# Kernel optimization log

Hardware: AMD Instinct MI355X
Metric: run time of the kernel (lower is better)

Reference implementation:

```python
import jax, jax.numpy as jnp
import numpy as np

T, B, X, F, Z, H = 64, 512, 784, 64, 64, 512


def _lin(v, W, b):
    return v @ W.T + b


def _gru(xt, h, Wih, Whh, bih, bhh):
    # PyTorch GRUCell gate math
    gi = xt @ Wih.T + bih
    gh = h @ Whh.T + bhh
    ir, iz, in_ = jnp.split(gi, 3, axis=-1)
    hr, hz, hn = jnp.split(gh, 3, axis=-1)
    r = jax.nn.sigmoid(ir + hr)
    z = jax.nn.sigmoid(iz + hz)
    n = jnp.tanh(in_ + r * hn)
    return (1.0 - z) * n + z * h


def _kld(mu1, sd1, mu2, sd2):
    r = sd1 / sd2
    return 0.5 * jnp.sum(((mu1 - mu2) / sd2) ** 2 + r ** 2 - 2.0 * jnp.log(r) - 1.0)


def setup_inputs() -> dict:
    key = jax.random.key(0)
    ks = iter(jax.random.split(key, 64))

    def Wn(*shape):
        return 0.02 * jax.random.normal(next(ks), shape, jnp.float32)

    d = {}
    d["x"] = jax.random.uniform(next(ks), (T, B, X), jnp.float32)
    d["eps_f"] = jax.random.normal(next(ks), (B, F), jnp.float32)
    d["eps_z"] = jax.random.normal(next(ks), (T, B, Z), jnp.float32)
    d.update(
        pxW1=Wn(H, X), pxb1=Wn(H), pxW2=Wn(H, H), pxb2=Wn(H),
        pzW=Wn(H, Z), pzb=Wn(H),
        pfW=Wn(H, F), pfb=Wn(H),
        rWih=Wn(3 * H, 3 * H), rWhh=Wn(3 * H, H), rbih=Wn(3 * H), rbhh=Wn(3 * H),
        zpW=Wn(H, H), zpb=Wn(H), zpmW=Wn(Z, H), zpmb=Wn(Z), zpsW=Wn(Z, H), zpsb=Wn(Z),
        feWih=Wn(3 * H, H), feWhh=Wn(3 * H, H), febih=Wn(3 * H), febhh=Wn(3 * H),
        femW=Wn(F, H), femb=Wn(F), fesW=Wn(F, H), fesb=Wn(F),
        zeW1=Wn(H, 2 * H), zeb1=Wn(H), zeW2=Wn(H, H), zeb2=Wn(H),
        zemW=Wn(Z, H), zemb=Wn(Z), zesW=Wn(Z, H), zesb=Wn(Z),
        dW1=Wn(H, 3 * H), db1=Wn(H), dW2=Wn(H, H), db2=Wn(H),
        dmW=Wn(X, H), dmb=Wn(X),
    )
    return d


def reference(x, eps_f, eps_z, pxW1, pxb1, pxW2, pxb2, pzW, pzb, pfW, pfb,
              rWih, rWhh, rbih, rbhh, zpW, zpb, zpmW, zpmb, zpsW, zpsb,
              feWih, feWhh, febih, febhh, femW, femb, fesW, fesb,
              zeW1, zeb1, zeW2, zeb2, zemW, zemb, zesW, zesb,
              dW1, db1, dW2, db2, dmW, dmb):
    relu = jax.nn.relu
    # phi_x over all timesteps at once: [T, B, H]
    phi_x = relu(_lin(relu(_lin(x, pxW1, pxb1)), pxW2, pxb2))
    h0 = jnp.zeros((x.shape[1], H), x.dtype)

    # f encoder GRU over the sequence; only the final hidden is used
    f_h, _ = jax.lax.scan(
        lambda h, xt: (_gru(xt, h, feWih, feWhh, febih, febhh), None), h0, phi_x)
    f_mean = _lin(f_h, femW, femb)
    f_std = jax.nn.softplus(_lin(f_h, fesW, fesb))
    f = eps_f * f_std + f_mean
    phi_f = relu(_lin(f, pfW, pfb))
    f_kld = _kld(f_mean, f_std, jnp.zeros_like(f_mean), jnp.ones_like(f_std))

    def step(carry, inp):
        h, zk, nll = carry
        px_t, e_t, x_t = inp
        zp = relu(_lin(h, zpW, zpb))
        zpm = _lin(zp, zpmW, zpmb)
        zps = jax.nn.softplus(_lin(zp, zpsW, zpsb))
        ze = relu(_lin(relu(_lin(jnp.concatenate([px_t, h], 1), zeW1, zeb1)), zeW2, zeb2))
        zem = _lin(ze, zemW, zemb)
        zes = jax.nn.softplus(_lin(ze, zesW, zesb))
        z_t = e_t * zes + zem
        phi_z = relu(_lin(z_t, pzW, pzb))
        dec = relu(_lin(relu(_lin(jnp.concatenate([phi_z, phi_f, h], 1), dW1, db1)), dW2, db2))
        dec_mean = jax.nn.sigmoid(_lin(dec, dmW, dmb))
        h_new = _gru(jnp.concatenate([px_t, phi_z, phi_f], 1), h, rWih, rWhh, rbih, rbhh)
        zk = zk + _kld(zem, zes, zpm, zps)
        nll = nll - jnp.sum(x_t * jnp.log(dec_mean) + (1.0 - x_t) * jnp.log(1.0 - dec_mean))
        return (h_new, zk, nll), None

    zero = jnp.zeros((), x.dtype)
    (_, z_kld, nll), _ = jax.lax.scan(step, (h0, zero, zero), (phi_x, eps_z, x))
    return (f_kld, z_kld, nll)
```

## Files before the change

### kernel.cpp

```cpp
#include <hip/hip_runtime.h>
#include <cmath>

namespace {

constexpr int Tn = 64;
constexpr int Bn = 512;
constexpr int Xn = 784;
constexpr int XnP = 800;
constexpr int Fn = 64;
constexpr int Zn = 64;
constexpr int Hn = 512;

typedef unsigned short us;
typedef __attribute__((ext_vector_type(8))) short bf16x8;
typedef __attribute__((ext_vector_type(4))) float f32x4;

__device__ __forceinline__ us f2b(float v) {
  unsigned int u = __float_as_uint(v);
  return (us)((u + 0x7FFFu + ((u >> 16) & 1u)) >> 16);
}
__device__ __forceinline__ float b2f(us u) { return __uint_as_float(((unsigned int)u) << 16); }
__device__ __forceinline__ float sigmf(float v) { return 1.0f / (1.0f + __expf(-v)); }
__device__ __forceinline__ float splusf(float v) {
  return v > 0.0f ? (v + log1pf(__expf(-v))) : log1pf(__expf(v));
}
__device__ __forceinline__ float block_sum(float v, float* red) {
  #pragma unroll
  for (int off = 32; off > 0; off >>= 1) v += __shfl_down(v, off, 64);
  if ((threadIdx.x & 63) == 0) red[threadIdx.x >> 6] = v;
  __syncthreads();
  float s = 0.0f;
  if (threadIdx.x == 0) s = red[0] + red[1] + red[2] + red[3];
  return s;
}

__global__ void cvt(const float* __restrict__ s, us* __restrict__ d, int n) {
  int i = blockIdx.x * 256 + threadIdx.x;
  if (i < n) d[i] = f2b(s[i]);
}
__global__ void cvt_pad(const float* __restrict__ s, us* __restrict__ d, int C, int Cp, int n) {
  int i = blockIdx.x * 256 + threadIdx.x;
  if (i < n) {
    int r = i / Cp, c = i - r * Cp;
    d[i] = (c < C) ? f2b(s[(size_t)r * C + c]) : (us)0;
  }
}

template <int NSEG, bool RELU, bool F32OUT, bool HASINIT, bool HASBIAS>
__device__ void tile_gemmx(
    int bx, int by,
    const us* A0, const us* W0, int ldw0, int K0,
    const us* A1, const us* W1, int ldw1, int K1,
    const float* initC, int ldi, const float* bias,
    void* Cout, int ldc, char* smemc)
{
  us* As = (us*)smemc; us* Bs = (us*)(smemc + 5120);
  const int tid = threadIdx.x, srow = tid >> 2, scb = (tid & 3) * 8;
  const int lane = tid & 63, w = tid >> 6, l15 = lane & 15, q = lane >> 4;
  const int m0 = by * 64, n0 = bx * 64;
  f32x4 acc[4];
  if (HASINIT) {
    #pragma unroll
    for (int j = 0; j < 4; ++j)
      #pragma unroll
      for (int r = 0; r < 4; ++r)
        acc[j][r] = initC[(size_t)(m0 + w * 16 + q * 4 + r) * ldi + n0 + j * 16 + l15];
  } else {
    #pragma unroll
    for (int j = 0; j < 4; ++j) acc[j] = (f32x4){0.f, 0.f, 0.f, 0.f};
  }
  #pragma unroll
  for (int seg = 0; seg < NSEG; ++seg) {
    const us* A = (seg == 0) ? A0 : A1;
    const us* W = (seg == 0) ? W0 : W1;
    const int ldw = (seg == 0) ? ldw0 : ldw1;
    const int K   = (seg == 0) ? K0 : K1;
    const us* ap = A + (size_t)(m0 + srow) * K + scb;
    const us* wp = W + (size_t)(n0 + srow) * ldw + scb;
    uint4 av = *(const uint4*)ap;
    uint4 wv = *(const uint4*)wp;
    for (int k0 = 0; k0 < K; k0 += 32) {
      __syncthreads();
      *(uint4*)&As[srow * 40 + scb] = av;
      *(uint4*)&Bs[srow * 40 + scb] = wv;
      __syncthreads();
      if (k0 + 32 < K) {
        av = *(const uint4*)(ap + k0 + 32);
        wv = *(const uint4*)(wp + k0 + 32);
      }
      bf16x8 a = *(const bf16x8*)&As[(w * 16 + l15) * 40 + q * 8];
      #pragma unroll
      for (int j = 0; j < 4; ++j) {
        bf16x8 b = *(const bf16x8*)&Bs[(j * 16 + l15) * 40 + q * 8];
        acc[j] = __builtin_amdgcn_mfma_f32_16x16x32_bf16(a, b, acc[j], 0, 0, 0);
      }
    }
  }
  #pragma unroll
  for (int j = 0; j < 4; ++j) {
    const int col = n0 + j * 16 + l15;
    const float bv = HASBIAS ? bias[col] : 0.f;
    #pragma unroll
    for (int r = 0; r < 4; ++r) {
      const int row = m0 + w * 16 + q * 4 + r;
      float v = acc[j][r] + bv;
      if (RELU) v = fmaxf(v, 0.f);
      if (F32OUT) ((float*)Cout)[(size_t)row * ldc + col] = v;
      else        ((us*)Cout)[(size_t)row * ldc + col] = f2b(v);
    }
  }
}

__device__ void tile_gru_fe(
    int bx, int by,
    const us* A0, const us* Wih,
    const us* hprev, const us* Whh,
    const float* bih, const float* bhh,
    us* hnew, char* smemc)
{
  us* Asm = (us*)smemc; us* Rs = (us*)(smemc + 5120);
  us* Zs = (us*)(smemc + 10240); us* Ns = (us*)(smemc + 15360);
  const int tid = threadIdx.x, srow = tid >> 2, scb = (tid & 3) * 8;
  const int lane = tid & 63, w = tid >> 6, l15 = lane & 15, q = lane >> 4;
  const int m0 = by * 64, c0 = bx * 64;
  f32x4 aR[4], aZ[4], aI[4], aH[4];
  #pragma unroll
  for (int j = 0; j < 4; ++j) {
    aR[j] = (f32x4){0.f, 0.f, 0.f, 0.f}; aZ[j] = aR[j]; aI[j] = aR[j]; aH[j] = aR[j];
  }
  #pragma unroll
  for (int seg = 0; seg < 2; ++seg) {
    const bool hseg = (seg == 1);
    const us* A  = hseg ? hprev : A0;
    const us* Wb = hseg ? Whh : Wih;
    const us* ap = A + (size_t)(m0 + srow) * Hn + scb;
    const us* wr = Wb + (size_t)(c0 + srow) * Hn + scb;
    const us* wz = wr + (size_t)Hn * Hn;
    const us* wn = wz + (size_t)Hn * Hn;
    uint4 av = *(const uint4*)ap;
    uint4 rv = *(const uint4*)wr;
    uint4 zv = *(const uint4*)wz;
    uint4 nv = *(const uint4*)wn;
    for (int k0 = 0; k0 < Hn; k0 += 32) {
      __syncthreads();
      *(uint4*)&Asm[srow * 40 + scb] = av;
      *(uint4*)&Rs[srow * 40 + scb] = rv;
      *(uint4*)&Zs[srow * 40 + scb] = zv;
      *(uint4*)&Ns[srow * 40 + scb] = nv;
      __syncthreads();
      if (k0 + 32 < Hn) {
        av = *(const uint4*)(ap + k0 + 32);
        rv = *(const uint4*)(wr + k0 + 32);
        zv = *(const uint4*)(wz + k0 + 32);
        nv = *(const uint4*)(wn + k0 + 32);
      }
      bf16x8 a = *(const bf16x8*)&Asm[(w * 16 + l15) * 40 + q * 8];
      #pragma unroll
      for (int j = 0; j < 4; ++j) {
        bf16x8 br = *(const bf16x8*)&Rs[(j * 16 + l15) * 40 + q * 8];
        bf16x8 bz = *(const bf16x8*)&Zs[(j * 16 + l15) * 40 + q * 8];
        bf16x8 bn = *(const bf16x8*)&Ns[(j * 16 + l15) * 40 + q * 8];
// ... 51 lines not shown
    }
  }
  const us* ap = phiz + (size_t)(m0 + srow) * Hn + scb;
  const us* wr = rWih + (size_t)(c0 + srow) * 1536 + 512 + scb;
  const us* wz = wr + (size_t)512 * 1536;
  const us* wn = wz + (size_t)512 * 1536;
  uint4 av = *(const uint4*)ap;
  uint4 rv = *(const uint4*)wr;
  uint4 zv = *(const uint4*)wz;
  uint4 nv = *(const uint4*)wn;
  for (int k0 = 0; k0 < Hn; k0 += 32) {
    __syncthreads();
    *(uint4*)&Asm[srow * 40 + scb] = av;
    *(uint4*)&Rs[srow * 40 + scb] = rv;
    *(uint4*)&Zs[srow * 40 + scb] = zv;
    *(uint4*)&Ns[srow * 40 + scb] = nv;
    __syncthreads();
    if (k0 + 32 < Hn) {
      av = *(const uint4*)(ap + k0 + 32);
      rv = *(const uint4*)(wr + k0 + 32);
      zv = *(const uint4*)(wz + k0 + 32);
      nv = *(const uint4*)(wn + k0 + 32);
    }
    bf16x8 a = *(const bf16x8*)&Asm[(w * 16 + l15) * 40 + q * 8];
    #pragma unroll
    for (int j = 0; j < 4; ++j) {
      bf16x8 br = *(const bf16x8*)&Rs[(j * 16 + l15) * 40 + q * 8];
      bf16x8 bz = *(const bf16x8*)&Zs[(j * 16 + l15) * 40 + q * 8];
      bf16x8 bn = *(const bf16x8*)&Ns[(j * 16 + l15) * 40 + q * 8];
      aR[j] = __builtin_amdgcn_mfma_f32_16x16x32_bf16(a, br, aR[j], 0, 0, 0);
      aZ[j] = __builtin_amdgcn_mfma_f32_16x16x32_bf16(a, bz, aZ[j], 0, 0, 0);
      aI[j] = __builtin_amdgcn_mfma_f32_16x16x32_bf16(a, bn, aI[j], 0, 0, 0);
    }
  }
  #pragma unroll
  for (int j = 0; j < 4; ++j) {
    const int c = c0 + j * 16 + l15;
    const float bR = bih[c] + bhh[c];
    const float bZ = bih[Hn + c] + bhh[Hn + c];
    const float bI = bih[2 * Hn + c];
    const float bH = bhh[2 * Hn + c];
    #pragma unroll
    for (int r = 0; r < 4; ++r) {
      const int m = m0 + w * 16 + q * 4 + r;
      const float h = b2f(hprev[(size_t)m * Hn + c]);
      const float rg = sigmf(aR[j][r] + bR);
      const float zg = sigmf(aZ[j][r] + bZ);
      const float ng = tanhf(aI[j][r] + bI + rg * (aH[j][r] + bH));
      hnew[(size_t)m * Hn + c] = f2b((1.0f - zg) * ng + zg * h);
    }
  }
}

__device__ void tile_nll(
    int bx, int by,
    const us* dec, const us* dmW, const float* dmb, const float* xt,
    float* nll, char* smemc)
{
  us* As = (us*)smemc; us* Bs = (us*)(smemc + 5120);
  float* red = (float*)(smemc + 10240);
  const int tid = threadIdx.x, srow = tid >> 2, scb = (tid & 3) * 8;
  const int lane = tid & 63, w = tid >> 6, l15 = lane & 15, q = lane >> 4;
  const int m0 = by * 64, n0 = bx * 64;
  f32x4 acc[4];
  #pragma unroll
  for (int j = 0; j < 4; ++j) acc[j] = (f32x4){0.f, 0.f, 0.f, 0.f};
  const int wrow = (n0 + srow < Xn) ? (n0 + srow) : (Xn - 1);
  const us* ap = dec + (size_t)(m0 + srow) * Hn + scb;
  const us* wp = dmW + (size_t)wrow * Hn + scb;
  uint4 av = *(const uint4*)ap;
  uint4 wv = *(const uint4*)wp;
  for (int k0 = 0; k0 < Hn; k0 += 32) {
    __syncthreads();
    *(uint4*)&As[srow * 40 + scb] = av;
    *(uint4*)&Bs[srow * 40 + scb] = wv;
    __syncthreads();
    if (k0 + 32 < Hn) {
      av = *(const uint4*)(ap + k0 + 32);
      wv = *(const uint4*)(wp + k0 + 32);
    }
    bf16x8 a = *(const bf16x8*)&As[(w * 16 + l15) * 40 + q * 8];
    #pragma unroll
    for (int j = 0; j < 4; ++j) {
      bf16x8 b = *(const bf16x8*)&Bs[(j * 16 + l15) * 40 + q * 8];
      acc[j] = __builtin_amdgcn_mfma_f32_16x16x32_bf16(a, b, acc[j], 0, 0, 0);
    }
  }
  float sum = 0.0f;
  #pragma unroll
  for (int j = 0; j < 4; ++j) {
    const int n = n0 + j * 16 + l15;
    if (n < Xn) {
      const float bv = dmb[n];
      #pragma unroll
      for (int r = 0; r < 4; ++r) {
        const int m = m0 + w * 16 + q * 4 + r;
        const float a = acc[j][r] + bv;
        const float xv = xt[(size_t)m * Xn + n];
        sum += splusf(-a) + (1.0f - xv) * a;
      }
    }
  }
  const float s = block_sum(sum, red);
  if (tid == 0) atomicAdd(nll, s);
}

template <int MODE>
__device__ void stat_dual(int vb,
    const us* Ain, const us* Wm, const float* bm, const us* Ws, const float* bs,
    const float* eps, const float* pm_in, const float* ps_in,
    us* o0b, float* o_pm, float* o_ps, float* kacc, char* smemc)
{
  us* As = (us*)smemc; us* Ms = (us*)(smemc + 5120); us* Ss = (us*)(smemc + 10240);
  float* red = (float*)(smemc + 15360);
  const int tid = threadIdx.x, srow = tid >> 2, scb = (tid & 3) * 8;
  const int lane = tid & 63, w = tid >> 6, l15 = lane & 15, q = lane >> 4;
  const int m0 = vb * 64;
  f32x4 am[4], as_[4];
  #pragma unroll
  for (int j = 0; j < 4; ++j) { am[j] = (f32x4){0.f, 0.f, 0.f, 0.f}; as_[j] = am[j]; }
  const us* ap = Ain + (size_t)(m0 + srow) * Hn + scb;
  const us* mp = Wm + (size_t)srow * Hn + scb;
  const us* sp = Ws + (size_t)srow * Hn + scb;
  uint4 av = *(const uint4*)ap;
  uint4 mv = *(const uint4*)mp;
  uint4 sv = *(const uint4*)sp;
  for (int k0 = 0; k0 < Hn; k0 += 32) {
    __syncthreads();
    *(uint4*)&As[srow * 40 + scb] = av;
    *(uint4*)&Ms[srow * 40 + scb] = mv;
    *(uint4*)&Ss[srow * 40 + scb] = sv;
    __syncthreads();
    if (k0 + 32 < Hn) {
      av = *(const uint4*)(ap + k0 + 32);
      mv = *(const uint4*)(mp + k0 + 32);
      sv = *(const uint4*)(sp + k0 + 32);
    }
    bf16x8 a = *(const bf16x8*)&As[(w * 16 + l15) * 40 + q * 8];
    #pragma unroll
    for (int j = 0; j < 4; ++j) {
      bf16x8 b0 = *(const bf16x8*)&Ms[(j * 16 + l15) * 40 + q * 8];
      bf16x8 b1 = *(const bf16x8*)&Ss[(j * 16 + l15) * 40 + q * 8];
      am[j]  = __builtin_amdgcn_mfma_f32_16x16x32_bf16(a, b0, am[j], 0, 0, 0);
      as_[j] = __builtin_amdgcn_mfma_f32_16x16x32_bf16(a, b1, as_[j], 0, 0, 0);
    }
  }
  float kld = 0.0f;
  #pragma unroll
  for (int j = 0; j < 4; ++j) {
    const int c = j * 16 + l15;
    const float bmv = bm[c], bsv = bs[c];
    #pragma unroll
    for (int r = 0; r < 4; ++r) {
      const int m = m0 + w * 16 + q * 4 + r;
      const float mu = am[j][r] + bmv;
      const float sd = splusf(as_[j][r] + bsv);
      if (MODE == 0) {
        o_pm[(size_t)m * Zn + c] = mu;
        o_ps[(size_t)m * Zn + c] = sd;
      } else {
        o0b[(size_t)m * Zn + c] = f2b(eps[(size_t)m * Zn + c] * sd + mu);
        if (MODE == 1) {
          kld += mu * mu + sd * sd - 2.0f * __logf(sd) - 1.0f;
        } else {
          const float pm = pm_in[(size_t)m * Zn + c];
          const float ps = ps_in[(size_t)m * Zn + c];
          const float dd = (mu - pm) / ps;
          const float rr = sd / ps;
          kld += dd * dd + rr * rr - 2.0f * __logf(rr) - 1.0f;
        }
      }
    }
  }
  if (MODE != 0) {
    const float s = block_sum(kld, red);
    if (tid == 0) atomicAdd(kacc, 0.5f * s);
  }
}

__global__ __launch_bounds__(256) void k_gemmA(
    const us* A, const us* W, int ldw, int K, const float* bias, us* C, int ldc)
{
  __shared__ alignas(16) char sm[10240];
  tile_gemmx<1, true, false, false, true>(blockIdx.x, blockIdx.y, A, W, ldw, K,
      nullptr, nullptr, 0, 0, nullptr, 0, bias, C, ldc, sm);
}

__global__ __launch_bounds__(256) void k_gruB(
    const us* A0, const us* Wih, const us* hprev, const us* Whh,
    const float* bih, const float* bhh, us* hnew)
{
  __shared__ alignas(16) char sm[20480];
  tile_gru_fe(blockIdx.x, blockIdx.y, A0, Wih, hprev, Whh, bih, bhh, hnew, sm);
}

__global__ __launch_bounds__(256) void k_statf(
    const us* fh, const us* femW, const float* femb, const us* fesW, const float* fesb,
    const float* eps_f, us* fbuf, float* kacc)
{
  __shared__ alignas(16) char sm[15376];
  stat_dual<1>(blockIdx.x, fh, femW, femb, fesW, fesb, eps_f,
               nullptr, nullptr, fbuf, nullptr, nullptr, kacc, sm);
}

__global__ __launch_bounds__(256) void kP2(
    const us* phi_f, const us* rWih, const us* dW1, const float* db1,
    float* Cpre_gru, float* Cpre_dec)
{
  __shared__ alignas(16) char sm[10240];
  const int b = blockIdx.x;
  if (b < 192)
    tile_gemmx<1, false, true, false, false>(b % 24, b / 24, phi_f, rWih + 1024, 1536, Hn,
        nullptr, nullptr, 0, 0, nullptr, 0, nullptr, Cpre_gru, 1536, sm);
  else
    tile_gemmx<1, false, true, false, true>((b - 192) & 7, (b - 192) >> 3,
        phi_f, dW1 + 512, 1536, Hn,
        nullptr, nullptr, 0, 0, nullptr, 0, db1, Cpre_dec, 512, sm);
}

__global__ __launch_bounds__(256) void kP3(
    const us* h0, const us* zpW, const float* zpb, us* zp,
    const us* px0, const us* zeW1, const float* zeb1, us* zepre)
{
  __shared__ alignas(16) char sm[10240];
  const int b = blockIdx.x;
  if (b < 64)
    tile_gemmx<1, true, false, false, true>(b & 7, b >> 3, h0, zpW, Hn, Hn,
        nullptr, nullptr, 0, 0, nullptr, 0, zpb, zp, Hn, sm);
  else
    tile_gemmx<2, true, false, false, true>((b - 64) & 7, (b - 64) >> 3,
        px0, zeW1, 1024, Hn, h0, zeW1 + 512, 1024, Hn,
        nullptr, 0, zeb1, zepre, Hn, sm);
}

__global__ __launch_bounds__(256) void kP4(
    const us* zepre, const us* zeW2, const float* zeb2, us* ze,
    const us* zp, const us* zpmW, const float* zpmb, const us* zpsW, const float* zpsb,
    float* zpm, float* zps)
{
  __shared__ alignas(16) char sm[15376];
  const int b = blockIdx.x;
  if (b < 64)
    tile_gemmx<1, true, false, false, true>(b & 7, b >> 3, zepre, zeW2, Hn, Hn,
        nullptr, nullptr, 0, 0, nullptr, 0, zeb2, ze, Hn, sm);
  else
    stat_dual<0>(b - 64, zp, zpmW, zpmb, zpsW, zpsb,
                 nullptr, nullptr, nullptr, nullptr, zpm, zps, nullptr, sm);
}

__global__ __launch_bounds__(256) void kS1(
    const us* ze, const us* zemW, const float* zemb, const us* zesW, const float* zesb,
    const float* eps_zt, const float* zpm, const float* zps, us* zt, float* kacc,
    const us* px_t, const us* rWih, const float* Cpre_gru, float* gipre)
{
  __shared__ alignas(16) char sm[15376];
  const int b = blockIdx.x;
  if (b < 8)
    stat_dual<2>(b, ze, zemW, zemb, zesW, zesb, eps_zt, zpm, zps,
                 zt, nullptr, nullptr, kacc, sm);
  else {
    const int tb = b - 8;
    tile_gemmx<1, false, true, true, false>(tb % 24, tb / 24, px_t, rWih, 1536, Hn,
        nullptr, nullptr, 0, 0, Cpre_gru, 1536, nullptr, gipre, 1536, sm);
  }
}

__global__ __launch_bounds__(256) void kS2(
    const us* zt, const us* pzW, const float* pzb, us* phiz)
{
  __shared__ alignas(16) char sm[10240];
  tile_gemmx<1, true, false, false, true>(blockIdx.x & 7, blockIdx.x >> 3, zt, pzW, Zn, Zn,
      nullptr, nullptr, 0, 0, nullptr, 0, pzb, phiz, Hn, sm);
}

__global__ __launch_bounds__(256) void kS3(
    const us* phiz, const us* rWih, const float* gipre, const float* ghpre,
    const us* hprev, const float* rbih, const float* rbhh, us* hnew,
    const us* dW1, const float* dtmph, us* dtmp)
{
  __shared__ alignas(16) char sm[20480];
  const int b = blockIdx.x;
  if (b < 64)
    tile_gru_fin(b & 7, b >> 3, phiz, rWih, gipre, ghpre, hprev, rbih, rbhh, hnew, sm);
  else
    tile_gemmx<1, true, false, true, false>((b - 64) & 7, (b - 64) >> 3, phiz, dW1, 1536, Hn,
        nullptr, nullptr, 0, 0, dtmph, 512, nullptr, dtmp, Hn, sm);
}

__global__ __launch_bounds__(256) void kS4(
    const us* dtmp, const us* dW2, const float* db2, us* dec,
    const us* hnext, const us* zpW, const float* zpb, us* zp,
    const us* px1, const us* zeW1, const float* zeb1, us* zepre,
    const us* dW1, const float* Cpre_dec, float* dtmph)
{
  __shared__ alignas(16) char sm[10240];
  const int b = blockIdx.x;
  if (b < 64)
    tile_gemmx<1, true, false, false, true>(b & 7, b >> 3, dtmp, dW2, Hn, Hn,
        nullptr, nullptr, 0, 0, nullptr, 0, db2, dec, Hn, sm);
  else if (b < 128)
    tile_gemmx<1, true, false, false, true>((b - 64) & 7, (b - 64) >> 3, hnext, zpW, Hn, Hn,
        nullptr, nullptr, 0, 0, nullptr, 0, zpb, zp, Hn, sm);
  else if (b < 192)
    tile_gemmx<2, true, false, false, true>((b - 128) & 7, (b - 128) >> 3,
        px1, zeW1, 1024, Hn, hnext, zeW1 + 512, 1024, Hn,
        nullptr, 0, zeb1, zepre, Hn, sm);
  else
    tile_gemmx<1, false, true, true, false>((b - 192) & 7, (b - 192) >> 3,
        hnext, dW1 + 1024, 1536, Hn,
        nullptr, nullptr, 0, 0, Cpre_dec, 512, nullptr, dtmph, 512, sm);
}

__global__ __launch_bounds__(256) void kS5(
    const us* dec, const us* dmW, const float* dmb, const float* xt, float* nll,
    const us* zepre, const us* zeW2, const float* zeb2, us* ze,
    const us* zp, const us* zpmW, const float* zpmb, const us* zpsW, const float* zpsb,
    float* zpm, float* zps,
    const us* hnext, const us* rWhh, float* ghpre)
{
  __shared__ alignas(16) char sm[15376];
  const int b = blockIdx.x;
  if (b < 104)
    tile_nll(b % 13, b / 13, dec, dmW, dmb, xt, nll, sm);
  else if (b < 168)
    tile_gemmx<1, true, false, false, true>((b - 104) & 7, (b - 104) >> 3, zepre, zeW2, Hn, Hn,
        nullptr, nullptr, 0, 0, nullptr, 0, zeb2, ze, Hn, sm);
  else if (b < 176)
    stat_dual<0>(b - 168, zp, zpmW, zpmb, zpsW, zpsb,
                 nullptr, nullptr, nullptr, nullptr, zpm, zps, nullptr, sm);
  else {
    const int tb = b - 176;
    tile_gemmx<1, false, true, false, false>(tb % 24, tb / 24, hnext, rWhh, Hn, Hn,
        nullptr, nullptr, 0, 0, nullptr, 0, nullptr, ghpre, 1536, sm);
  }
}

}

extern "C" void kernel_launch(void* const* d_in, const int* in_sizes, int n_in,
                              void* d_out, int out_size, void* d_ws, size_t ws_size,
                              hipStream_t stream)
{
  (void)in_sizes; (void)n_in; (void)out_size;
  const float* x     = (const float*)d_in[0];
  const float* eps_f = (const float*)d_in[1];
  const float* eps_z = (const float*)d_in[2];
  const float* pxW1  = (const float*)d_in[3];
  const float* pxb1  = (const float*)d_in[4];
  const float* pxW2  = (const float*)d_in[5];
  const float* pxb2  = (const float*)d_in[6];
  const float* pzW   = (const float*)d_in[7];
  const float* pzb   = (const float*)d_in[8];
  const float* pfW   = (const float*)d_in[9];
  const float* pfb   = (const float*)d_in[10];
  const float* rWih  = (const float*)d_in[11];
  const float* rWhh  = (const float*)d_in[12];
  const float* rbih  = (const float*)d_in[13];
  const float* rbhh  = (const float*)d_in[14];
  const float* zpW   = (const float*)d_in[15];
  const float* zpb   = (const float*)d_in[16];
  const float* zpmW  = (const float*)d_in[17];
  const float* zpmb  = (const float*)d_in[18];
  const float* zpsW  = (const float*)d_in[19];
  const float* zpsb  = (const float*)d_in[20];
  const float* feWih = (const float*)d_in[21];
  const float* feWhh = (const float*)d_in[22];
  const float* febih = (const float*)d_in[23];
  const float* febhh = (const float*)d_in[24];
  const float* femW  = (const float*)d_in[25];
  const float* femb  = (const float*)d_in[26];
  const float* fesW  = (const float*)d_in[27];
  const float* fesb  = (const float*)d_in[28];
  const float* zeW1  = (const float*)d_in[29];
  const float* zeb1  = (const float*)d_in[30];
  const float* zeW2  = (const float*)d_in[31];
  const float* zeb2  = (const float*)d_in[32];
  const float* zemW  = (const float*)d_in[33];
  const float* zemb  = (const float*)d_in[34];
  const float* zesW  = (const float*)d_in[35];
  const float* zesb  = (const float*)d_in[36];
  const float* dW1   = (const float*)d_in[37];
  const float* db1   = (const float*)d_in[38];
  const float* dW2   = (const float*)d_in[39];
  const float* db2   = (const float*)d_in[40];
  const float* dmW   = (const float*)d_in[41];
  const float* dmb   = (const float*)d_in[42];
  float* out = (float*)d_out;

  char* base = (char*)d_ws;
  size_t off = 0;
  auto ab = [&](size_t bytes) -> void* {
    void* p = base + off;
    off += (bytes + 255) & ~(size_t)255;
    return p;
  };

  us* b_pxW1  = (us*)ab((size_t)512 * XnP * 2);
  us* b_pxW2  = (us*)ab((size_t)512 * 512 * 2);
  us* b_pzW   = (us*)ab((size_t)512 * 64 * 2);
  us* b_pfW   = (us*)ab((size_t)512 * 64 * 2);
  us* b_rWih  = (us*)ab((size_t)1536 * 1536 * 2);
  us* b_rWhh  = (us*)ab((size_t)1536 * 512 * 2);
  us* b_zpW   = (us*)ab((size_t)512 * 512 * 2);
  us* b_zpmW  = (us*)ab((size_t)64 * 512 * 2);
  us* b_zpsW  = (us*)ab((size_t)64 * 512 * 2);
  us* b_feWih = (us*)ab((size_t)1536 * 512 * 2);
  us* b_feWhh = (us*)ab((size_t)1536 * 512 * 2);
  us* b_femW  = (us*)ab((size_t)64 * 512 * 2);
  us* b_fesW  = (us*)ab((size_t)64 * 512 * 2);
  us* b_zeW1  = (us*)ab((size_t)512 * 1024 * 2);
  us* b_zeW2  = (us*)ab((size_t)512 * 512 * 2);
  us* b_zemW  = (us*)ab((size_t)64 * 512 * 2);
  us* b_zesW  = (us*)ab((size_t)64 * 512 * 2);
  us* b_dW1   = (us*)ab((size_t)512 * 1536 * 2);
  us* b_dW2   = (us*)ab((size_t)512 * 512 * 2);
  us* b_dmW   = (us*)ab((size_t)Xn * 512 * 2);

  us* phi_x = (us*)ab((size_t)Tn * Bn * Hn * 2);
  us* fh_a  = (us*)ab((size_t)Bn * Hn * 2);
  us* h_a   = (us*)ab((size_t)Bn * Hn * 2);
  us* fh_b  = (us*)ab((size_t)Bn * Hn * 2);
  us* h_b   = (us*)ab((size_t)Bn * Hn * 2);
  us* fbuf  = (us*)ab((size_t)Bn * Fn * 2);
  us* phi_f = (us*)ab((size_t)Bn * Hn * 2);
  us* zp    = (us*)ab((size_t)Bn * Hn * 2);
  us* zepre = (us*)ab((size_t)Bn * Hn * 2);
  us* ze    = (us*)ab((size_t)Bn * Hn * 2);
  us* zt    = (us*)ab((size_t)Bn * Zn * 2);
  us* phiz  = (us*)ab((size_t)Bn * Hn * 2);
  us* dtmp  = (us*)ab((size_t)Bn * Hn * 2);
  us* dec   = (us*)ab((size_t)Bn * Hn * 2);
  float* zpm = (float*)ab((size_t)Bn * Zn * 4);
  float* zps = (float*)ab((size_t)Bn * Zn * 4);
  float* Cpre_gru = (float*)ab((size_t)Bn * 1536 * 4);
  float* Cpre_dec = (float*)ab((size_t)Bn * 512 * 4);
  float* gipre    = (float*)ab((size_t)Bn * 1536 * 4);
  float* ghpre    = (float*)ab((size_t)Bn * 1536 * 4);
  float* dtmph    = (float*)ab((size_t)Bn * 512 * 4);

  int CH = 16;
  while (CH > 1 && off + (size_t)CH * (Bn * XnP + Bn * Hn) * 2 + 4096 > ws_size) CH >>= 1;
  us* xch  = (us*)ab((size_t)CH * Bn * XnP * 2);
  us* tmpb = (us*)ab((size_t)CH * Bn * Hn * 2);

  hipMemsetAsync(d_out, 0, 3 * sizeof(float), stream);
  hipMemsetAsync(fh_a, 0, 2 * (size_t)Bn * Hn * 2, stream);
  hipMemsetAsync(ghpre, 0, (size_t)Bn * 1536 * 4, stream);

  const dim3 blk(256);
  auto CVT = [&](const float* s, us* d, size_t n) {
    cvt<<<dim3((unsigned)((n + 255) / 256)), blk, 0, stream>>>(s, d, (int)n);
  };

  {
    const size_t n = (size_t)512 * XnP;
    cvt_pad<<<dim3((unsigned)((n + 255) / 256)), blk, 0, stream>>>(pxW1, b_pxW1, Xn, XnP, (int)n);
  }
  CVT(pxW2, b_pxW2, (size_t)512 * 512);
  CVT(pzW, b_pzW, (size_t)512 * 64);
  CVT(pfW, b_pfW, (size_t)512 * 64);
  CVT(rWih, b_rWih, (size_t)1536 * 1536);
  CVT(rWhh, b_rWhh, (size_t)1536 * 512);
  CVT(zpW, b_zpW, (size_t)512 * 512);
  CVT(zpmW, b_zpmW, (size_t)64 * 512);
  CVT(zpsW, b_zpsW, (size_t)64 * 512);
  CVT(feWih, b_feWih, (size_t)1536 * 512);
  CVT(feWhh, b_feWhh, (size_t)1536 * 512);
  CVT(femW, b_femW, (size_t)64 * 512);
  CVT(fesW, b_fesW, (size_t)64 * 512);
  CVT(zeW1, b_zeW1, (size_t)512 * 1024);
  CVT(zeW2, b_zeW2, (size_t)512 * 512);
  CVT(zemW, b_zemW, (size_t)64 * 512);
  CVT(zesW, b_zesW, (size_t)64 * 512);
  CVT(dW1, b_dW1, (size_t)512 * 1536);
  CVT(dW2, b_dW2, (size_t)512 * 512);
  CVT(dmW, b_dmW, (size_t)Xn * 512);

  for (int c = 0; c < Tn / CH; ++c) {
    const size_t nx = (size_t)CH * Bn * XnP;
    cvt_pad<<<dim3((unsigned)((nx + 255) / 256)), blk, 0, stream>>>(
        x + (size_t)c * CH * Bn * Xn, xch, Xn, XnP, (int)nx);
    const dim3 gA(8, CH * Bn / 64);
    k_gemmA<<<gA, blk, 0, stream>>>(xch, b_pxW1, XnP, XnP, pxb1, tmpb, Hn);
    k_gemmA<<<gA, blk, 0, stream>>>(tmpb, b_pxW2, Hn, Hn, pxb2,
                                    phi_x + (size_t)c * CH * Bn * Hn, Hn);
  }

  us* fc = fh_a; us* fn2 = fh_b;
  for (int t = 0; t < Tn; ++t) {
    k_gruB<<<dim3(8, 8), blk, 0, stream>>>(
        phi_x + (size_t)t * Bn * Hn, b_feWih, fc, b_feWhh, febih, febhh, fn2);
    us* sw = fc; fc = fn2; fn2 = sw;
  }

  k_statf<<<dim3(8), blk, 0, stream>>>(fh_a, b_femW, femb, b_fesW, fesb, eps_f, fbuf, out + 0);

  k_gemmA<<<dim3(8, 8), blk, 0, stream>>>(fbuf, b_pfW, Fn, Fn, pfb, phi_f, Hn);
  kP2<<<dim3(256), blk, 0, stream>>>(phi_f, b_rWih, b_dW1, db1, Cpre_gru, Cpre_dec);
  hipMemcpyAsync(dtmph, Cpre_dec, (size_t)Bn * 512 * 4, hipMemcpyDeviceToDevice, stream);
  kP3<<<dim3(128), blk, 0, stream>>>(h_a, b_zpW, zpb, zp, phi_x, b_zeW1, zeb1, zepre);
  kP4<<<dim3(72), blk, 0, stream>>>(zepre, b_zeW2, zeb2, ze,
                                    zp, b_zpmW, zpmb, b_zpsW, zpsb, zpm, zps);

  for (int t = 0; t < Tn; ++t) {
    const us* hcur = (t & 1) ? h_b : h_a;
    us* hnext      = (t & 1) ? h_a : h_b;
    const bool last = (t == Tn - 1);
    const us* px_t = phi_x + (size_t)t * Bn * Hn;

    kS1<<<dim3(200), blk, 0, stream>>>(
        ze, b_zemW, zemb, b_zesW, zesb, eps_z + (size_t)t * Bn * Zn, zpm, zps,
        zt, out + 1, px_t, b_rWih, Cpre_gru, gipre);

    kS2<<<dim3(64), blk, 0, stream>>>(zt, b_pzW, pzb, phiz);

    kS3<<<dim3(128), blk, 0, stream>>>(
        phiz, b_rWih, gipre, ghpre, hcur, rbih, rbhh, hnext,
        b_dW1, dtmph, dtmp);

    kS4<<<dim3(last ? 64 : 256), blk, 0, stream>>>(
        dtmp, b_dW2, db2, dec,
        hnext, b_zpW, zpb, zp,
        phi_x + (size_t)(t + 1) * Bn * Hn, b_zeW1, zeb1, zepre,
        b_dW1, Cpre_dec, dtmph);

    kS5<<<dim3(last ? 104 : 368), blk, 0, stream>>>(
        dec, b_dmW, dmb, x + (size_t)t * Bn * Xn, out + 2,
        zepre, b_zeW2, zeb2, ze,
        zp, b_zpmW, zpmb, b_zpsW, zpsb, zpm, zps,
        hnext, b_rWhh, ghpre);
  }
}
```

Measured before the change: 6.594 ms.

## Fuse recurrent step kernels and defer NLL decoder head to one batched kernel

Merges the 19 weight-conversion launches into one grid-stride kernel. Fuses the z posterior stats with the phi_z projection, and computes the three GRU gates in one tile with a shared A load. Removes the per-step NLL tiles from the recurrence: each step's decoder output is stored into the already consumed phi_x slot, and a single large kernel evaluates all timesteps' NLL after the loop. The memcpy is dropped by reading Cpre_dec directly at t=0. This cuts launches and serial per-step work in exchange for reusing the phi_x buffer and running fewer, larger blocks in some steps.

```diff
diff --git a/kernel.cpp b/kernel.cpp
--- a/kernel.cpp
+++ b/kernel.cpp
@@ -34,11 +34,28 @@
   return s;
 }
 
-__global__ void cvt(const float* __restrict__ s, us* __restrict__ d, int n) {
-  int i = blockIdx.x * 256 + threadIdx.x;
-  if (i < n) d[i] = f2b(s[i]);
-}
-__global__ void cvt_pad(const float* __restrict__ s, us* __restrict__ d, int C, int Cp, int n) {
+struct CvtP {
+  const float* s[19];
+  us* d[19];
+  int n[19];
+  const float* pxW1src;
+  us* pxW1dst;
+};
+__global__ __launch_bounds__(256) void k_cvt_all(CvtP p) {
+  const int gtid = blockIdx.x * 256 + threadIdx.x;
+  const int gnt = gridDim.x * 256;
+  for (int k = 0; k < 19; ++k) {
+    const float* s = p.s[k]; us* d = p.d[k]; const int n = p.n[k];
+    for (int i = gtid; i < n; i += gnt) d[i] = f2b(s[i]);
+  }
+  for (int i = gtid; i < 512 * XnP; i += gnt) {
+    const int r = i / XnP, c = i - r * XnP;
+    p.pxW1dst[i] = (c < Xn) ? f2b(p.pxW1src[(size_t)r * Xn + c]) : (us)0;
+  }
+}
+
+__global__ __launch_bounds__(256) void cvt_pad(
+    const float* __restrict__ s, us* __restrict__ d, int C, int Cp, int n) {
   int i = blockIdx.x * 256 + threadIdx.x;
   if (i < n) {
     int r = i / Cp, c = i - r * Cp;
@@ -107,6 +124,79 @@
       if (RELU) v = fmaxf(v, 0.f);
       if (F32OUT) ((float*)Cout)[(size_t)row * ldc + col] = v;
       else        ((us*)Cout)[(size_t)row * ldc + col] = f2b(v);
+    }
+  }
+}
+
+template <bool HASINIT>
+__device__ void tile_g3(int bx, int by, const us* A, const us* W, int ldw,
+                        const float* initC, float* outC, char* smemc)
+{
+  us* Asm = (us*)smemc; us* Rs = (us*)(smemc + 5120);
+  us* Zs = (us*)(smemc + 10240); us* Ns = (us*)(smemc + 15360);
+  const int tid = threadIdx.x, srow = tid >> 2, scb = (tid & 3) * 8;
+  const int lane = tid & 63, w = tid >> 6, l15 = lane & 15, q = lane >> 4;
+  const int m0 = by * 64, c0 = bx * 64;
+  f32x4 aR[4], aZ[4], aN[4];
+  if (HASINIT) {
+    #pragma unroll
+    for (int j = 0; j < 4; ++j) {
+      const int c = c0 + j * 16 + l15;
+      #pragma unroll
+      for (int r = 0; r < 4; ++r) {
+        const size_t row = (size_t)(m0 + w * 16 + q * 4 + r) * 1536;
+        aR[j][r] = initC[row + c];
+        aZ[j][r] = initC[row + 512 + c];
+        aN[j][r] = initC[row + 1024 + c];
+      }
+    }
+  } else {
+    #pragma unroll
+    for (int j = 0; j < 4; ++j) {
+      aR[j] = (f32x4){0.f, 0.f, 0.f, 0.f}; aZ[j] = aR[j]; aN[j] = aR[j];
+    }
+  }
+  const us* ap = A + (size_t)(m0 + srow) * Hn + scb;
+  const us* wr = W + (size_t)(c0 + srow) * ldw + scb;
+  const us* wz = wr + (size_t)512 * ldw;
+  const us* wn = wz + (size_t)512 * ldw;
+  uint4 av = *(const uint4*)ap;
+  uint4 rv = *(const uint4*)wr;
+  uint4 zv = *(const uint4*)wz;
+  uint4 nv = *(const uint4*)wn;
+  for (int k0 = 0; k0 < Hn; k0 += 32) {
+    __syncthreads();
+    *(uint4*)&Asm[srow * 40 + scb] = av;
+    *(uint4*)&Rs[srow * 40 + scb] = rv;
+    *(uint4*)&Zs[srow * 40 + scb] = zv;
+    *(uint4*)&Ns[srow * 40 + scb] = nv;
+    __syncthreads();
+    if (k0 + 32 < Hn) {
+      av = *(const uint4*)(ap + k0 + 32);
+      rv = *(const uint4*)(wr + k0 + 32);
+      zv = *(const uint4*)(wz + k0 + 32);
+      nv = *(const uint4*)(wn + k0 + 32);
+    }
+    bf16x8 a = *(const bf16x8*)&Asm[(w * 16 + l15) * 40 + q * 8];
+    #pragma unroll
+    for (int j = 0; j < 4; ++j) {
+      bf16x8 br = *(const bf16x8*)&Rs[(j * 16 + l15) * 40 + q * 8];
+      bf16x8 bz = *(const bf16x8*)&Zs[(j * 16 + l15) * 40 + q * 8];
+      bf16x8 bn = *(const bf16x8*)&Ns[(j * 16 + l15) * 40 + q * 8];
+      aR[j] = __builtin_amdgcn_mfma_f32_16x16x32_bf16(a, br, aR[j], 0, 0, 0);
+      aZ[j] = __builtin_amdgcn_mfma_f32_16x16x32_bf16(a, bz, aZ[j], 0, 0, 0);
+      aN[j] = __builtin_amdgcn_mfma_f32_16x16x32_bf16(a, bn, aN[j], 0, 0, 0);
+    }
+  }
+  #pragma unroll
+  for (int j = 0; j < 4; ++j) {
+    const int c = c0 + j * 16 + l15;
+    #pragma unroll
+    for (int r = 0; r < 4; ++r) {
+      const size_t row = (size_t)(m0 + w * 16 + q * 4 + r) * 1536;
+      outC[row + c] = aR[j][r];
+      outC[row + 512 + c] = aZ[j][r];
+      outC[row + 1024 + c] = aN[j][r];
     }
   }
 }
@@ -264,63 +354,10 @@
   }
 }
 
-__device__ void tile_nll(
-    int bx, int by,
-    const us* dec, const us* dmW, const float* dmb, const float* xt,
-    float* nll, char* smemc)
-{
-  us* As = (us*)smemc; us* Bs = (us*)(smemc + 5120);
-  float* red = (float*)(smemc + 10240);
-  const int tid = threadIdx.x, srow = tid >> 2, scb = (tid & 3) * 8;
-  const int lane = tid & 63, w = tid >> 6, l15 = lane & 15, q = lane >> 4;
-  const int m0 = by * 64, n0 = bx * 64;
-  f32x4 acc[4];
-  #pragma unroll
-  for (int j = 0; j < 4; ++j) acc[j] = (f32x4){0.f, 0.f, 0.f, 0.f};
-  const int wrow = (n0 + srow < Xn) ? (n0 + srow) : (Xn - 1);
-  const us* ap = dec + (size_t)(m0 + srow) * Hn + scb;
-  const us* wp = dmW + (size_t)wrow * Hn + scb;
-  uint4 av = *(const uint4*)ap;
-  uint4 wv = *(const uint4*)wp;
-  for (int k0 = 0; k0 < Hn; k0 += 32) {
-    __syncthreads();
-    *(uint4*)&As[srow * 40 + scb] = av;
-    *(uint4*)&Bs[srow * 40 + scb] = wv;
-    __syncthreads();
-    if (k0 + 32 < Hn) {
-      av = *(const uint4*)(ap + k0 + 32);
-      wv = *(const uint4*)(wp + k0 + 32);
-    }
-    bf16x8 a = *(const bf16x8*)&As[(w * 16 + l15) * 40 + q * 8];
-    #pragma unroll
-    for (int j = 0; j < 4; ++j) {
-      bf16x8 b = *(const bf16x8*)&Bs[(j * 16 + l15) * 40 + q * 8];
-      acc[j] = __builtin_amdgcn_mfma_f32_16x16x32_bf16(a, b, acc[j], 0, 0, 0);
-    }
-  }
-  float sum = 0.0f;
-  #pragma unroll
-  for (int j = 0; j < 4; ++j) {
-    const int n = n0 + j * 16 + l15;
-    if (n < Xn) {
-      const float bv = dmb[n];
-      #pragma unroll
-      for (int r = 0; r < 4; ++r) {
-        const int m = m0 + w * 16 + q * 4 + r;
-        const float a = acc[j][r] + bv;
-        const float xv = xt[(size_t)m * Xn + n];
-        sum += splusf(-a) + (1.0f - xv) * a;
-      }
-    }
-  }
-  const float s = block_sum(sum, red);
-  if (tid == 0) atomicAdd(nll, s);
-}
-
 template <int MODE>
 __device__ void stat_dual(int vb,
     const us* Ain, const us* Wm, const float* bm, const us* Ws, const float* bs,
-    const float* eps, const float* pm_in, const float* ps_in,
+    const float* eps,
     us* o0b, float* o_pm, float* o_ps, float* kacc, char* smemc)
 {
   us* As = (us*)smemc; us* Ms = (us*)(smemc + 5120); us* Ss = (us*)(smemc + 10240);
@@ -372,15 +409,7 @@
         o_ps[(size_t)m * Zn + c] = sd;
       } else {
         o0b[(size_t)m * Zn + c] = f2b(eps[(size_t)m * Zn + c] * sd + mu);
-        if (MODE == 1) {
-          kld += mu * mu + sd * sd - 2.0f * __logf(sd) - 1.0f;
-        } else {
-          const float pm = pm_in[(size_t)m * Zn + c];
-          const float ps = ps_in[(size_t)m * Zn + c];
-          const float dd = (mu - pm) / ps;
-          const float rr = sd / ps;
-          kld += dd * dd + rr * rr - 2.0f * __logf(rr) - 1.0f;
-        }
+        kld += mu * mu + sd * sd - 2.0f * __logf(sd) - 1.0f;
       }
     }
   }
@@ -390,6 +419,105 @@
   }
 }
 
+__device__ void tile_zestat_phiz(int vb,
+    const us* ze, const us* Wm, const float* bm, const us* Ws, const float* bs,
+    const float* eps, const float* pm_in, const float* ps_in,
+    const us* pzW, const float* pzb, us* phiz,
+    float* kacc, char* smemc)
+{
+  us* As = (us*)smemc; us* Ms = (us*)(smemc + 5120); us* Ss = (us*)(smemc + 10240);
+  float* red = (float*)(smemc + 15360);
+  const int tid = threadIdx.x, srow = tid >> 2, scb = (tid & 3) * 8;
+  const int lane = tid & 63, w = tid >> 6, l15 = lane & 15, q = lane >> 4;
+  const int m0 = vb * 64;
+  f32x4 am[4], as_[4];
+  #pragma unroll
+  for (int j = 0; j < 4; ++j) { am[j] = (f32x4){0.f, 0.f, 0.f, 0.f}; as_[j] = am[j]; }
+  const us* ap = ze + (size_t)(m0 + srow) * Hn + scb;
+  const us* mp = Wm + (size_t)srow * Hn + scb;
+  const us* sp = Ws + (size_t)srow * Hn + scb;
+  uint4 av = *(const uint4*)ap;
+  uint4 mv = *(const uint4*)mp;
+  uint4 sv = *(const uint4*)sp;
+  for (int k0 = 0; k0 < Hn; k0 += 32) {
+    __syncthreads();
+    *(uint4*)&As[srow * 40 + scb] = av;
+    *(uint4*)&Ms[srow * 40 + scb] = mv;
+    *(uint4*)&Ss[srow * 40 + scb] = sv;
+    __syncthreads();
+    if (k0 + 32 < Hn) {
+      av = *(const uint4*)(ap + k0 + 32);
+      mv = *(const uint4*)(mp + k0 + 32);
+      sv = *(const uint4*)(sp + k0 + 32);
+    }
+    bf16x8 a = *(const bf16x8*)&As[(w * 16 + l15) * 40 + q * 8];
+    #pragma unroll
+    for (int j = 0; j < 4; ++j) {
+      bf16x8 b0 = *(const bf16x8*)&Ms[(j * 16 + l15) * 40 + q * 8];
+      bf16x8 b1 = *(const bf16x8*)&Ss[(j * 16 + l15) * 40 + q * 8];
+      am[j]  = __builtin_amdgcn_mfma_f32_16x16x32_bf16(a, b0, am[j], 0, 0, 0);
+      as_[j] = __builtin_amdgcn_mfma_f32_16x16x32_bf16(a, b1, as_[j], 0, 0, 0);
+    }
+  }
+  float kld = 0.0f;
+  us ztv[4][4];
+  #pragma unroll
+  for (int j = 0; j < 4; ++j) {
+    const int c = j * 16 + l15;
+    const float bmv = bm[c], bsv = bs[c];
+    #pragma unroll
+    for (int r = 0; r < 4; ++r) {
+      const int m = m0 + w * 16 + q * 4 + r;
+      const float mu = am[j][r] + bmv;
+      const float sd = splusf(as_[j][r] + bsv);
+      ztv[j][r] = f2b(eps[(size_t)m * Zn + c] * sd + mu);
+      const float pm = pm_in[(size_t)m * Zn + c];
+      const float ps = ps_in[(size_t)m * Zn + c];
+      const float dd = (mu - pm) / ps;
+      const float rr = sd / ps;
+      kld += dd * dd + rr * rr - 2.0f * __logf(rr) - 1.0f;
+    }
+  }
+  const float s = block_sum(kld, red);
+  if (tid == 0) atomicAdd(kacc, 0.5f * s);
+  us* zts = (us*)smemc;
+  us* Bs = (us*)(smemc + 10240);
+  #pragma unroll
+  for (int j = 0; j < 4; ++j)
+    #pragma unroll
+    for (int r = 0; r < 4; ++r)
+      zts[(w * 16 + q * 4 + r) * 72 + (j * 16 + l15)] = ztv[j][r];
+  for (int nt = 0; nt < 8; ++nt) {
+    f32x4 pa[4];
+    #pragma unroll
+    for (int j = 0; j < 4; ++j) pa[j] = (f32x4){0.f, 0.f, 0.f, 0.f};
+    const us* wp = pzW + (size_t)(nt * 64 + srow) * 64 + scb;
+    uint4 wv = *(const uint4*)wp;
+    for (int k0 = 0; k0 < 64; k0 += 32) {
+      __syncthreads();
+      *(uint4*)&Bs[srow * 40 + scb] = wv;
+      __syncthreads();
+      if (k0 == 0) wv = *(const uint4*)(wp + 32);
+      bf16x8 a = *(const bf16x8*)&zts[(w * 16 + l15) * 72 + k0 + q * 8];
+      #pragma unroll
+      for (int j = 0; j < 4; ++j) {
+        bf16x8 b = *(const bf16x8*)&Bs[(j * 16 + l15) * 40 + q * 8];
+        pa[j] = __builtin_amdgcn_mfma_f32_16x16x32_bf16(a, b, pa[j], 0, 0, 0);
+      }
+    }
+    #pragma unroll
+    for (int j = 0; j < 4; ++j) {
+      const int col = nt * 64 + j * 16 + l15;
+      const float bv = pzb[col];
+      #pragma unroll
+      for (int r = 0; r < 4; ++r) {
+        const int row = m0 + w * 16 + q * 4 + r;
+        phiz[(size_t)row * Hn + col] = f2b(fmaxf(pa[j][r] + bv, 0.f));
+      }
+    }
+  }
+}
+
 __global__ __launch_bounds__(256) void k_gemmA(
     const us* A, const us* W, int ldw, int K, const float* bias, us* C, int ldc)
 {
@@ -412,20 +540,19 @@
 {
   __shared__ alignas(16) char sm[15376];
   stat_dual<1>(blockIdx.x, fh, femW, femb, fesW, fesb, eps_f,
-               nullptr, nullptr, fbuf, nullptr, nullptr, kacc, sm);
+               fbuf, nullptr, nullptr, kacc, sm);
 }
 
 __global__ __launch_bounds__(256) void kP2(
     const us* phi_f, const us* rWih, const us* dW1, const float* db1,
     float* Cpre_gru, float* Cpre_dec)
 {
-  __shared__ alignas(16) char sm[10240];
+  __shared__ alignas(16) char sm[20480];
   const int b = blockIdx.x;
-  if (b < 192)
-    tile_gemmx<1, false, true, false, false>(b % 24, b / 24, phi_f, rWih + 1024, 1536, Hn,
-        nullptr, nullptr, 0, 0, nullptr, 0, nullptr, Cpre_gru, 1536, sm);
+  if (b < 64)
+    tile_g3<false>(b & 7, b >> 3, phi_f, rWih + 1024, 1536, nullptr, Cpre_gru, sm);
   else
-    tile_gemmx<1, false, true, false, true>((b - 192) & 7, (b - 192) >> 3,
+    tile_gemmx<1, false, true, false, true>((b - 64) & 7, (b - 64) >> 3,
         phi_f, dW1 + 512, 1536, Hn,
         nullptr, nullptr, 0, 0, nullptr, 0, db1, Cpre_dec, 512, sm);
 }
@@ -457,35 +584,25 @@
         nullptr, nullptr, 0, 0, nullptr, 0, zeb2, ze, Hn, sm);
   else
     stat_dual<0>(b - 64, zp, zpmW, zpmb, zpsW, zpsb,
-                 nullptr, nullptr, nullptr, nullptr, zpm, zps, nullptr, sm);
-}
-
-__global__ __launch_bounds__(256) void kS1(
+                 nullptr, nullptr, zpm, zps, nullptr, sm);
+}
+
+__global__ __launch_bounds__(256) void kD1(
     const us* ze, const us* zemW, const float* zemb, const us* zesW, const float* zesb,
-    const float* eps_zt, const float* zpm, const float* zps, us* zt, float* kacc,
+    const float* eps_zt, const float* zpm, const float* zps,
+    const us* pzW, const float* pzb, us* phiz, float* kacc,
     const us* px_t, const us* rWih, const float* Cpre_gru, float* gipre)
 {
-  __shared__ alignas(16) char sm[15376];
+  __shared__ alignas(16) char sm[20480];
   const int b = blockIdx.x;
   if (b < 8)
-    stat_dual<2>(b, ze, zemW, zemb, zesW, zesb, eps_zt, zpm, zps,
-                 zt, nullptr, nullptr, kacc, sm);
-  else {
-    const int tb = b - 8;
-    tile_gemmx<1, false, true, true, false>(tb % 24, tb / 24, px_t, rWih, 1536, Hn,
-        nullptr, nullptr, 0, 0, Cpre_gru, 1536, nullptr, gipre, 1536, sm);
-  }
-}
-
-__global__ __launch_bounds__(256) void kS2(
-    const us* zt, const us* pzW, const float* pzb, us* phiz)
-{
-  __shared__ alignas(16) char sm[10240];
-  tile_gemmx<1, true, false, false, true>(blockIdx.x & 7, blockIdx.x >> 3, zt, pzW, Zn, Zn,
-      nullptr, nullptr, 0, 0, nullptr, 0, pzb, phiz, Hn, sm);
-}
-
-__global__ __launch_bounds__(256) void kS3(
+    tile_zestat_phiz(b, ze, zemW, zemb, zesW, zesb, eps_zt, zpm, zps,
+                     pzW, pzb, phiz, kacc, sm);
+  else
+    tile_g3<true>((b - 8) & 7, (b - 8) >> 3, px_t, rWih, 1536, Cpre_gru, gipre, sm);
+}
+
+__global__ __launch_bounds__(256) void kD2(
     const us* phiz, const us* rWih, const float* gipre, const float* ghpre,
     const us* hprev, const float* rbih, const float* rbhh, us* hnew,
     const us* dW1, const float* dtmph, us* dtmp)
@@ -499,8 +616,8 @@
         nullptr, nullptr, 0, 0, dtmph, 512, nullptr, dtmp, Hn, sm);
 }
 
-__global__ __launch_bounds__(256) void kS4(
-    const us* dtmp, const us* dW2, const float* db2, us* dec,
+__global__ __launch_bounds__(256) void kD3(
+    const us* dtmp, const us* dW2, const float* db2, us* dec_slot,
     const us* hnext, const us* zpW, const float* zpb, us* zp,
     const us* px1, const us* zeW1, const float* zeb1, us* zepre,
     const us* dW1, const float* Cpre_dec, float* dtmph)
@@ -509,7 +626,7 @@
   const int b = blockIdx.x;
   if (b < 64)
     tile_gemmx<1, true, false, false, true>(b & 7, b >> 3, dtmp, dW2, Hn, Hn,
-        nullptr, nullptr, 0, 0, nullptr, 0, db2, dec, Hn, sm);
+        nullptr, nullptr, 0, 0, nullptr, 0, db2, dec_slot, Hn, sm);
   else if (b < 128)
     tile_gemmx<1, true, false, false, true>((b - 64) & 7, (b - 64) >> 3, hnext, zpW, Hn, Hn,
         nullptr, nullptr, 0, 0, nullptr, 0, zpb, zp, Hn, sm);
@@ -523,28 +640,81 @@
         nullptr, nullptr, 0, 0, Cpre_dec, 512, nullptr, dtmph, 512, sm);
 }
 
-__global__ __launch_bounds__(256) void kS5(
-    const us* dec, const us* dmW, const float* dmb, const float* xt, float* nll,
+__global__ __launch_bounds__(256) void kD4(
     const us* zepre, const us* zeW2, const float* zeb2, us* ze,
     const us* zp, const us* zpmW, const float* zpmb, const us* zpsW, const float* zpsb,
     float* zpm, float* zps,
     const us* hnext, const us* rWhh, float* ghpre)
 {
-  __shared__ alignas(16) char sm[15376];
+  __shared__ alignas(16) char sm[20480];
   const int b = blockIdx.x;
-  if (b < 104)
-    tile_nll(b % 13, b / 13, dec, dmW, dmb, xt, nll, sm);
-  else if (b < 168)
-    tile_gemmx<1, true, false, false, true>((b - 104) & 7, (b - 104) >> 3, zepre, zeW2, Hn, Hn,
+  if (b < 64)
+    tile_gemmx<1, true, false, false, true>(b & 7, b >> 3, zepre, zeW2, Hn, Hn,
         nullptr, nullptr, 0, 0, nullptr, 0, zeb2, ze, Hn, sm);
-  else if (b < 176)
-    stat_dual<0>(b - 168, zp, zpmW, zpmb, zpsW, zpsb,
-                 nullptr, nullptr, nullptr, nullptr, zpm, zps, nullptr, sm);
-  else {
-    const int tb = b - 176;
-    tile_gemmx<1, false, true, false, false>(tb % 24, tb / 24, hnext, rWhh, Hn, Hn,
-        nullptr, nullptr, 0, 0, nullptr, 0, nullptr, ghpre, 1536, sm);
-  }
+  else if (b < 72)
+    stat_dual<0>(b - 64, zp, zpmW, zpmb, zpsW, zpsb,
+                 nullptr, nullptr, zpm, zps, nullptr, sm);
+  else
+    tile_g3<false>((b - 72) & 7, (b - 72) >> 3, hnext, rWhh, Hn, nullptr, ghpre, sm);
+}
+
+__global__ __launch_bounds__(256) void k_nll_all(
+    const us* dec_all, const us* dmW, const float* dmb, const float* x, float* nll)
+{
+  __shared__ alignas(16) char smemc[10256];
+  const int b = blockIdx.x;
+  const int t = b / 104;
+  const int i = b - t * 104;
+  const int bx = i % 13, by = i / 13;
+  const us* dec = dec_all + (size_t)t * Bn * Hn;
+  const float* xt = x + (size_t)t * Bn * Xn;
+
+  us* As = (us*)smemc; us* Bs = (us*)(smemc + 5120);
+  float* red = (float*)(smemc + 10240);
+  const int tid = threadIdx.x, srow = tid >> 2, scb = (tid & 3) * 8;
+  const int lane = tid & 63, w = tid >> 6, l15 = lane & 15, q = lane >> 4;
+  const int m0 = by * 64, n0 = bx * 64;
+  f32x4 acc[4];
+  #pragma unroll
+  for (int j = 0; j < 4; ++j) acc[j] = (f32x4){0.f, 0.f, 0.f, 0.f};
+  const int wrow = (n0 + srow < Xn) ? (n0 + srow) : (Xn - 1);
+  const us* ap = dec + (size_t)(m0 + srow) * Hn + scb;
+  const us* wp = dmW + (size_t)wrow * Hn + scb;
+  uint4 av = *(const uint4*)ap;
+  uint4 wv = *(const uint4*)wp;
+  for (int k0 = 0; k0 < Hn; k0 += 32) {
+    __syncthreads();
+    *(uint4*)&As[srow * 40 + scb] = av;
+    *(uint4*)&Bs[srow * 40 + scb] = wv;
+    __syncthreads();
+    if (k0 + 32 < Hn) {
+      av = *(const uint4*)(ap + k0 + 32);
+      wv = *(const uint4*)(wp + k0 + 32);
+    }
+    bf16x8 a = *(const bf16x8*)&As[(w * 16 + l15) * 40 + q * 8];
+    #pragma unroll
+    for (int j = 0; j < 4; ++j) {
+      bf16x8 bb = *(const bf16x8*)&Bs[(j * 16 + l15) * 40 + q * 8];
+      acc[j] = __builtin_amdgcn_mfma_f32_16x16x32_bf16(a, bb, acc[j], 0, 0, 0);
+    }
+  }
+  float sum = 0.0f;
+  #pragma unroll
+  for (int j = 0; j < 4; ++j) {
+    const int n = n0 + j * 16 + l15;
+    if (n < Xn) {
+      const float bv = dmb[n];
+      #pragma unroll
+      for (int r = 0; r < 4; ++r) {
+        const int m = m0 + w * 16 + q * 4 + r;
+        const float a = acc[j][r] + bv;
+        const float xv = xt[(size_t)m * Xn + n];
+        sum += splusf(-a) + (1.0f - xv) * a;
+      }
+    }
+  }
+  const float s = block_sum(sum, red);
+  if (tid == 0) atomicAdd(nll, s);
 }
 
 }
@@ -638,10 +808,8 @@
   us* zp    = (us*)ab((size_t)Bn * Hn * 2);
   us* zepre = (us*)ab((size_t)Bn * Hn * 2);
   us* ze    = (us*)ab((size_t)Bn * Hn * 2);
-  us* zt    = (us*)ab((size_t)Bn * Zn * 2);
   us* phiz  = (us*)ab((size_t)Bn * Hn * 2);
   us* dtmp  = (us*)ab((size_t)Bn * Hn * 2);
-  us* dec   = (us*)ab((size_t)Bn * Hn * 2);
   float* zpm = (float*)ab((size_t)Bn * Zn * 4);
   float* zps = (float*)ab((size_t)Bn * Zn * 4);
   float* Cpre_gru = (float*)ab((size_t)Bn * 1536 * 4);
@@ -660,33 +828,21 @@
   hipMemsetAsync(ghpre, 0, (size_t)Bn * 1536 * 4, stream);
 
   const dim3 blk(256);
-  auto CVT = [&](const float* s, us* d, size_t n) {
-    cvt<<<dim3((unsigned)((n + 255) / 256)), blk, 0, stream>>>(s, d, (int)n);
-  };
 
   {
-    const size_t n = (size_t)512 * XnP;
-    cvt_pad<<<dim3((unsigned)((n + 255) / 256)), blk, 0, stream>>>(pxW1, b_pxW1, Xn, XnP, (int)n);
-  }
-  CVT(pxW2, b_pxW2, (size_t)512 * 512);
-  CVT(pzW, b_pzW, (size_t)512 * 64);
-  CVT(pfW, b_pfW, (size_t)512 * 64);
-  CVT(rWih, b_rWih, (size_t)1536 * 1536);
-  CVT(rWhh, b_rWhh, (size_t)1536 * 512);
-  CVT(zpW, b_zpW, (size_t)512 * 512);
-  CVT(zpmW, b_zpmW, (size_t)64 * 512);
-  CVT(zpsW, b_zpsW, (size_t)64 * 512);
-  CVT(feWih, b_feWih, (size_t)1536 * 512);
-  CVT(feWhh, b_feWhh, (size_t)1536 * 512);
-  CVT(femW, b_femW, (size_t)64 * 512);
-  CVT(fesW, b_fesW, (size_t)64 * 512);
-  CVT(zeW1, b_zeW1, (size_t)512 * 1024);
-  CVT(zeW2, b_zeW2, (size_t)512 * 512);
-  CVT(zemW, b_zemW, (size_t)64 * 512);
-  CVT(zesW, b_zesW, (size_t)64 * 512);
-  CVT(dW1, b_dW1, (size_t)512 * 1536);
-  CVT(dW2, b_dW2, (size_t)512 * 512);
-  CVT(dmW, b_dmW, (size_t)Xn * 512);
+    CvtP cp;
+    const float* srcs[19] = {pxW2, pzW, pfW, rWih, rWhh, zpW, zpmW, zpsW,
+        feWih, feWhh, femW, fesW, zeW1, zeW2, zemW, zesW, dW1, dW2, dmW};
+    us* dsts[19] = {b_pxW2, b_pzW, b_pfW, b_rWih, b_rWhh, b_zpW, b_zpmW, b_zpsW,
+        b_feWih, b_feWhh, b_femW, b_fesW, b_zeW1, b_zeW2, b_zemW, b_zesW,
+        b_dW1, b_dW2, b_dmW};
+    const int ns[19] = {512*512, 512*64, 512*64, 1536*1536, 1536*512,
+        512*512, 64*512, 64*512, 1536*512, 1536*512, 64*512, 64*512,
+        512*1024, 512*512, 64*512, 64*512, 512*1536, 512*512, 784*512};
+    for (int k = 0; k < 19; ++k) { cp.s[k] = srcs[k]; cp.d[k] = dsts[k]; cp.n[k] = ns[k]; }
+    cp.pxW1src = pxW1; cp.pxW1dst = b_pxW1;
+    k_cvt_all<<<dim3(1024), blk, 0, stream>>>(cp);
+  }
 
   for (int c = 0; c < Tn / CH; ++c) {
     const size_t nx = (size_t)CH * Bn * XnP;
@@ -708,8 +864,7 @@
   k_statf<<<dim3(8), blk, 0, stream>>>(fh_a, b_femW, femb, b_fesW, fesb, eps_f, fbuf, out + 0);
 
   k_gemmA<<<dim3(8, 8), blk, 0, stream>>>(fbuf, b_pfW, Fn, Fn, pfb, phi_f, Hn);
-  kP2<<<dim3(256), blk, 0, stream>>>(phi_f, b_rWih, b_dW1, db1, Cpre_gru, Cpre_dec);
-  hipMemcpyAsync(dtmph, Cpre_dec, (size_t)Bn * 512 * 4, hipMemcpyDeviceToDevice, stream);
+  kP2<<<dim3(128), blk, 0, stream>>>(phi_f, b_rWih, b_dW1, db1, Cpre_gru, Cpre_dec);
   kP3<<<dim3(128), blk, 0, stream>>>(h_a, b_zpW, zpb, zp, phi_x, b_zeW1, zeb1, zepre);
   kP4<<<dim3(72), blk, 0, stream>>>(zepre, b_zeW2, zeb2, ze,
                                     zp, b_zpmW, zpmb, b_zpsW, zpsb, zpm, zps);
@@ -720,26 +875,26 @@
     const bool last = (t == Tn - 1);
     const us* px_t = phi_x + (size_t)t * Bn * Hn;
 
-    kS1<<<dim3(200), blk, 0, stream>>>(
+    kD1<<<dim3(72), blk, 0, stream>>>(
         ze, b_zemW, zemb, b_zesW, zesb, eps_z + (size_t)t * Bn * Zn, zpm, zps,
-        zt, out + 1, px_t, b_rWih, Cpre_gru, gipre);
-
-    kS2<<<dim3(64), blk, 0, stream>>>(zt, b_pzW, pzb, phiz);
-
-    kS3<<<dim3(128), blk, 0, stream>>>(
+        b_pzW, pzb, phiz, out + 1, px_t, b_rWih, Cpre_gru, gipre);
+
+    kD2<<<dim3(128), blk, 0, stream>>>(
         phiz, b_rWih, gipre, ghpre, hcur, rbih, rbhh, hnext,
-        b_dW1, dtmph, dtmp);
-
-    kS4<<<dim3(last ? 64 : 256), blk, 0, stream>>>(
-        dtmp, b_dW2, db2, dec,
+        b_dW1, (t == 0 ? Cpre_dec : dtmph), dtmp);
+
+    kD3<<<dim3(last ? 64 : 256), blk, 0, stream>>>(
+        dtmp, b_dW2, db2, phi_x + (size_t)t * Bn * Hn,
         hnext, b_zpW, zpb, zp,
         phi_x + (size_t)(t + 1) * Bn * Hn, b_zeW1, zeb1, zepre,
         b_dW1, Cpre_dec, dtmph);
 
-    kS5<<<dim3(last ? 104 : 368), blk, 0, stream>>>(
-        dec, b_dmW, dmb, x + (size_t)t * Bn * Xn, out + 2,
-        zepre, b_zeW2, zeb2, ze,
-        zp, b_zpmW, zpmb, b_zpsW, zpsb, zpm, zps,
-        hnext, b_rWhh, ghpre);
-  }
-}
+    if (!last)
+      kD4<<<dim3(136), blk, 0, stream>>>(
+          zepre, b_zeW2, zeb2, ze,
+          zp, b_zpmW, zpmb, b_zpsW, zpsb, zpm, zps,
+          hnext, b_rWhh, ghpre);
+  }
+
+  k_nll_all<<<dim3(Tn * 104), blk, 0, stream>>>(phi_x, b_dmW, dmb, x, out + 2);
+}
```

Result: slower. 6.963 ms (+5.6%).
